# Performance work log

Hardware: AMD Instinct MI355X
Metric: run time of the kernel (lower is better)

The kernel has to match this reference:

```python
import jax, jax.numpy as jnp
import numpy as np

B, S, F_IN = 8, 4096, 256      # batch, frames, mel bins
C = 256                        # model_complexity (out_features of attention)
G = 8                          # n_heads (groups)
K = 31                         # w_size (local window, odd)
F_OUT = 88                     # output_features (piano keys)
PAD = (K - 1) // 2


def setup_inputs() -> dict:
    key = jax.random.key(0)
    ks = jax.random.split(key, 7)
    s = 0.05
    return {
        "spec": jax.random.normal(ks[0], (B, S, F_IN), jnp.float32),
        "W_q": jax.random.normal(ks[1], (F_IN, C), jnp.float32) * s,
        "W_k": jax.random.normal(ks[2], (F_IN, C), jnp.float32) * s,
        "W_v": jax.random.normal(ks[3], (F_IN, C), jnp.float32) * s,
        "rel": jax.random.normal(ks[4], (C, K), jnp.float32),
        "W_lin": jax.random.normal(ks[5], (C, F_OUT), jnp.float32) * s,
        "b_lin": jax.random.normal(ks[6], (F_OUT,), jnp.float32) * s,
    }


def reference(spec, W_q, W_k, W_v, rel, W_lin, b_lin):
    b, s, _ = spec.shape
    d = C // G  # per-head dim
    # QKV projections (no bias, as in the module)
    q = spec @ W_q                                             # [B,S,C]
    padded = jnp.pad(spec, ((0, 0), (PAD, PAD), (0, 0)))       # [B,S+2p,F]
    k = padded @ W_k                                           # [B,S+2p,C]
    v = padded @ W_v
    # unfold: window index [S,K]
    idx = jnp.arange(s)[:, None] + jnp.arange(K)[None, :]      # [S,K]
    kw = jnp.transpose(k[:, idx, :], (0, 1, 3, 2))             # [B,S,C,K]
    vw = jnp.transpose(v[:, idx, :], (0, 1, 3, 2))             # [B,S,C,K]
    kw = kw + rel                                              # positional bias [C,K]
    kw = kw.reshape(b, s, G, d, K)
    vw = vw.reshape(b, s, G, d, K)
    qh = q.reshape(b, s, G, d)
    energy = jnp.einsum('bsgd,bsgdk->bsgk', qh, kw)            # [B,S,G,K]
    attn = jax.nn.softmax(energy, axis=-1)                     # [B,S,G,K]
    out = jnp.einsum('bsgk,bsgdk->bsgd', attn, vw).reshape(b, s, C)
    frame_pred = jax.nn.sigmoid(out @ W_lin + b_lin)           # [B,S,F_OUT]
    return frame_pred, attn
```

## Files before the change

kernel.cpp:

```cpp
#include <hip/hip_runtime.h>
#include <hip/hip_bf16.h>
#include <math.h>

#define B_   8
#define S_   4096
#define FIN  256
#define C_   256
#define G_   8
#define D_   32
#define K_   31
#define PAD_ 15
#define FOUT 88

typedef __bf16 bf16;
typedef __attribute__((ext_vector_type(8))) __bf16 bf16x8;
typedef __attribute__((ext_vector_type(4))) __bf16 bf16x4;
typedef __attribute__((ext_vector_type(4))) float f32x4;

#define MFMA16(A, B, C) __builtin_amdgcn_mfma_f32_16x16x32_bf16(A, B, C, 0, 0, 0)

__global__ __launch_bounds__(256) void prep_all(
    const float* __restrict__ Wq, const float* __restrict__ Wk,
    const float* __restrict__ Wv, const float* __restrict__ Wl,
    const float* __restrict__ rel,
    bf16* __restrict__ bth, bf16* __restrict__ btl,
    bf16* __restrict__ wlh, bf16* __restrict__ wll,
    bf16* __restrict__ Vt,
    bf16* __restrict__ relH, bf16* __restrict__ relL)
{
    const int bid = blockIdx.x;
    const int t   = threadIdx.x;

    if (bid < 768) {
        const int w = bid >> 8;
        const int k = bid & 255;
        const float* W = (w == 0) ? Wq : (w == 1) ? Wk : Wv;
        const float x = W[(size_t)k * 256 + t];
        const bf16 h = (bf16)x;
        const size_t o = (size_t)w * 65536 + (size_t)t * 256 + k;
        bth[o] = h;
        btl[o] = (bf16)(x - (float)h);
    } else if (bid < 896) {
        const int k = (bid - 768) * 2 + (t >> 7);
        const int n = t & 127;
        const float x = (n < FOUT) ? Wl[(size_t)k * FOUT + n] : 0.f;
        const bf16 h = (bf16)x;
        wlh[(size_t)n * 256 + k] = h;
        wll[(size_t)n * 256 + k] = (bf16)(x - (float)h);
    } else if (bid < 1024) {
        const int idx = (bid - 896) * 256 + t;
        const int bd  = idx >> 4;
        const int pos = (idx & 15) * 4;
        const int off = (pos < 16) ? pos : 4096 + pos;
        bf16x4 z = {};
        *(bf16x4*)&Vt[(size_t)bd * 4160 + off] = z;
    } else {
        const int idx = (bid - 1024) * 256 + t;
        const int g = idx >> 10, k = (idx >> 5) & 31, d = idx & 31;
        const float v = (k < 31) ? rel[(size_t)(g * 32 + d) * 31 + k] : 0.f;
        const bf16 h = (bf16)v;
        relH[idx] = h;
        relL[idx] = (bf16)(v - (float)h);
    }
}

__device__ __forceinline__ void gload16(const bf16* g, bf16* l) {
    __builtin_amdgcn_global_load_lds(
        (const __attribute__((address_space(1))) void*)g,
        (__attribute__((address_space(3))) void*)l, 16, 0, 0);
}

__device__ __forceinline__ void stage_tile(const bf16* g, bf16* l, int t) {
    const int lg = ((t & 3) ^ ((t >> 3) & 3)) * 8;
    const int r0 = t >> 2;
    const int r1 = 64 + (t >> 2);
    const int u0 = (t & ~63) * 8;
    gload16(g + (size_t)r0 * 256 + lg, l + u0);
    gload16(g + (size_t)r1 * 256 + lg, l + u0 + 2048);
}

__device__ __forceinline__ bf16x8 frag_ld(const bf16* l, int r, int cl) {
    return *(const bf16x8*)&l[r * 32 + ((cl ^ ((r >> 1) & 3)) << 3)];
}

__global__ __launch_bounds__(256) void qkv_mfma(
    const float* __restrict__ spec,
    const bf16* __restrict__ bth, const bf16* __restrict__ btl,
    bf16* __restrict__ Qh, bf16* __restrict__ Ql,
    bf16* __restrict__ Kh, bf16* __restrict__ Kl,
    bf16* __restrict__ Vt)
{
    __shared__ bf16 lds[4 * 4096];

    const int t   = threadIdx.x;
    const int swz = ((blockIdx.x & 7) * 192) + (blockIdx.x >> 3);
    const int mt  = swz / 6, nt = swz % 6;
    const int wt  = nt >> 1;
    const int m0  = mt * 128, n0 = (nt & 1) * 128;
    const bool three = (wt < 2);

    const float* a_g = spec + (size_t)m0 * 256;
    const bf16* bh_g = bth + (size_t)wt * 65536 + (size_t)n0 * 256;
    const bf16* bl_g = btl + (size_t)wt * 65536 + (size_t)n0 * 256;

    const int ar  = t >> 1;
    const int ak  = (t & 1) * 16;
    const int as_ = (ar >> 1) & 3;
    const int cc0 = ak >> 3;
    bf16* AhW0 = lds +        ar * 32 + (( cc0      ^ as_) << 3);
    bf16* AhW1 = lds +        ar * 32 + (((cc0 + 1) ^ as_) << 3);
    bf16* AlW0 = lds + 4096 + ar * 32 + (( cc0      ^ as_) << 3);
    bf16* AlW1 = lds + 4096 + ar * 32 + (((cc0 + 1) ^ as_) << 3);
    const float* aRow = a_g + (size_t)ar * 256 + ak;

    const int lane = t & 63, wid = t >> 6;
    const int wr = (wid >> 1) * 64, wc = (wid & 1) * 64;
    const int fr = lane & 15, cl = lane >> 4;

    f32x4 acc[4][4];
#pragma unroll
    for (int m = 0; m < 4; ++m)
#pragma unroll
        for (int n = 0; n < 4; ++n)
            acc[m][n] = (f32x4){0.f, 0.f, 0.f, 0.f};

    for (int ks = 0; ks < 8; ++ks) {
        const int ko = ks * 32;

        const f32x4 a0 = *(const f32x4*)(aRow + ko);
        const f32x4 a1 = *(const f32x4*)(aRow + ko + 4);
        const f32x4 a2 = *(const f32x4*)(aRow + ko + 8);
        const f32x4 a3 = *(const f32x4*)(aRow + ko + 12);
        stage_tile(bh_g + ko, lds + 8192, t);
        stage_tile(bl_g + ko, lds + 12288, t);

        bf16x8 h0, h1, l0, l1;
#pragma unroll
        for (int j = 0; j < 4; ++j) {
            const bf16 x0 = (bf16)a0[j], x1 = (bf16)a1[j];
            const bf16 x2 = (bf16)a2[j], x3 = (bf16)a3[j];
            h0[j] = x0; h0[4 + j] = x1;
            h1[j] = x2; h1[4 + j] = x3;
            l0[j]     = (bf16)(a0[j] - (float)x0);
            l0[4 + j] = (bf16)(a1[j] - (float)x1);
            l1[j]     = (bf16)(a2[j] - (float)x2);
            l1[4 + j] = (bf16)(a3[j] - (float)x3);
        }
        *(bf16x8*)AhW0 = h0;
        *(bf16x8*)AhW1 = h1;
        if (three) {
            *(bf16x8*)AlW0 = l0;
            *(bf16x8*)AlW1 = l1;
        }
        __syncthreads();

        bf16x8 ah[4], bh8[4], bl8[4];
#pragma unroll
        for (int m = 0; m < 4; ++m) ah[m] = frag_ld(lds, wr + m * 16 + fr, cl);
#pragma unroll
        for (int n = 0; n < 4; ++n) {
            bh8[n] = frag_ld(lds + 8192,  wc + n * 16 + fr, cl);
            bl8[n] = frag_ld(lds + 12288, wc + n * 16 + fr, cl);
        }
#pragma unroll
        for (int m = 0; m < 4; ++m)
#pragma unroll
            for (int n = 0; n < 4; ++n) {
                acc[m][n] = MFMA16(ah[m], bh8[n], acc[m][n]);
                acc[m][n] = MFMA16(ah[m], bl8[n], acc[m][n]);
            }
        if (three) {
            bf16x8 al[4];
#pragma unroll
            for (int m = 0; m < 4; ++m) al[m] = frag_ld(lds + 4096, wr + m * 16 + fr, cl);
#pragma unroll
            for (int m = 0; m < 4; ++m)
#pragma unroll
                for (int n = 0; n < 4; ++n)
                    acc[m][n] = MFMA16(al[m], bh8[n], acc[m][n]);
        }
        __syncthreads();
    }

    if (wt < 2) {
        bf16* Oh = (wt == 0) ? Qh : Kh;
        bf16* Ol = (wt == 0) ? Ql : Kl;
#pragma unroll
        for (int m = 0; m < 4; ++m) {
            const int gr = m0 + wr + m * 16 + cl * 4;
#pragma unroll
            for (int n = 0; n < 4; ++n) {
                const int gc = n0 + wc + n * 16 + fr;
#pragma unroll
                for (int i = 0; i < 4; ++i) {
                    const float v = acc[m][n][i];
                    const bf16 hh = (bf16)v;
                    const size_t off = (size_t)(gr + i) * 256 + gc;
                    Oh[off] = hh;
                    Ol[off] = (bf16)(v - (float)hh);
                }
            }
        }
    } else {
#pragma unroll
        for (int m = 0; m < 4; ++m) {
            const int gr = m0 + wr + m * 16 + cl * 4;
            const int bb = gr >> 12, sr = gr & 4095;
#pragma unroll
            for (int n = 0; n < 4; ++n) {
                const int gc = n0 + wc + n * 16 + fr;
                bf16x4 pk;
#pragma unroll
                for (int i = 0; i < 4; ++i) pk[i] = (bf16)acc[m][n][i];
                *(bf16x4*)&Vt[(size_t)(bb * 256 + gc) * 4160 + 16 + sr] = pk;
            }
        }
    }
}

__global__ __launch_bounds__(256) void attn_mfma(
    const bf16* __restrict__ Qh, const bf16* __restrict__ Ql,
    const bf16* __restrict__ Kh, const bf16* __restrict__ Kl,
    const bf16* __restrict__ Vt,
    const bf16* __restrict__ relH, const bf16* __restrict__ relL,
    float* __restrict__ attn, bf16* __restrict__ Obf)
{
    __shared__ char ldsb[18432];

    const int t    = threadIdx.x;
    const int wid  = t >> 6;
    const int lane = t & 63;
    const int fr   = lane & 15;
    const int q    = lane >> 4;
    const int f7   = fr & 7;
    const int sl   = lane >> 2;
    const int jj   = lane & 3;

    const int bid2 = ((blockIdx.x & 7) << 8) | (blockIdx.x >> 3);
    const int sg0  = bid2 << 4;
    const int b    = sg0 >> 12;
    const int s0   = sg0 & 4095;

    float* Rbuf = (float*)(ldsb + wid * 4608);
    float* Pf32 = Rbuf;
    bf16*  Pbuf = (bf16*) (ldsb + wid * 4608 + 2304);

    {
        uint* p32 = (uint*)Pbuf;
#pragma unroll
        for (int j = 0; j < 9; ++j) p32[lane + 64 * j] = 0u;
    }

    const size_t rowQ = (size_t)(sg0 + fr) * 256;

#pragma unroll
    for (int h = 0; h < 2; ++h) {
        asm volatile("" ::: "memory");
        const int g   = wid * 2 + h;
        const int dof = g * 32 + q * 8;

        const bf16x8 qh8 = *(const bf16x8*)&Qh[rowQ + dof];
        const bf16x8 ql8 = *(const bf16x8*)&Ql[rowQ + dof];

        f32x4 e0, e1, e2;
#pragma unroll
        for (int tau = 0; tau < 3; ++tau) {
            const int trel = s0 - 16 + tau * 16 + fr;
            bf16x8 kh8 = {}, kl8 = {};
            if ((unsigned)trel < 4096u) {
                const size_t rk = ((size_t)(b << 12) + trel) * 256 + dof;
                kh8 = *(const bf16x8*)&Kh[rk];
                kl8 = *(const bf16x8*)&Kl[rk];
            }
            f32x4 a = (f32x4){0.f, 0.f, 0.f, 0.f};
            a = MFMA16(kh8, qh8, a);
            a = MFMA16(kh8, ql8, a);
            a = MFMA16(kl8, qh8, a);
            if (tau == 0) e0 = a; else if (tau == 1) e1 = a; else e2 = a;
        }

#pragma unroll
        for (int kap = 0; kap < 2; ++kap) {
            const size_t ro = (size_t)(g * 32 + kap * 16 + fr) * 32 + q * 8;
            const bf16x8 rh8 = *(const bf16x8*)&relH[ro];
            const bf16x8 rl8 = *(const bf16x8*)&relL[ro];
            f32x4 rc = (f32x4){0.f, 0.f, 0.f, 0.f};
            rc = MFMA16(rh8, qh8, rc);
            rc = MFMA16(rh8, ql8, rc);
            rc = MFMA16(rl8, qh8, rc);
#pragma unroll
            for (int r = 0; r < 4; ++r)
                Rbuf[(kap * 16 + q * 4 + r) * 18 + fr] = rc[r];
        }

        float ev[3][4];
        float mx = -3.0e38f;
#pragma unroll
        for (int tau = 0; tau < 3; ++tau) {
#pragma unroll
            for (int r = 0; r < 4; ++r) {
                const int rp = q * 4 + r;
                const int kk = tau * 16 + rp - fr - 1;
                const float eb = (tau == 0) ? e0[r] : (tau == 1) ? e1[r] : e2[r];
                float v = eb + Rbuf[(kk & 31) * 18 + fr];
                const bool valid = (tau == 1) || ((tau == 0) ? (rp > fr) : (rp < fr));
                v = valid ? v : -3.0e38f;
                ev[tau][r] = v;
                mx = fmaxf(mx, v);
            }
        }
        mx = fmaxf(mx, __shfl_xor(mx, 16));
        mx = fmaxf(mx, __shfl_xor(mx, 32));
        float sum = 0.f;
#pragma unroll
        for (int tau = 0; tau < 3; ++tau)
#pragma unroll
            for (int r = 0; r < 4; ++r) {
                const float p = __expf(ev[tau][r] - mx);
                ev[tau][r] = p;
                sum += p;
            }
        sum += __shfl_xor(sum, 16);
        sum += __shfl_xor(sum, 32);
        const float inv = 1.f / sum;

#pragma unroll
        for (int tau = 0; tau < 3; ++tau)
#pragma unroll
            for (int r = 0; r < 4; ++r) {
                const int rp = q * 4 + r;
                const int kk = tau * 16 + rp - fr - 1;
                const bool valid = (tau == 1) || ((tau == 0) ? (rp > fr) : (rp < fr));
                if (valid) {
                    const float p = ev[tau][r] * inv;
                    Pf32[fr * 36 + kk] = p;
                    const int tl = tau * 16 + rp;
                    Pbuf[fr * 72 + (((tl >> 3) ^ f7) << 3) + (tl & 7)] = (bf16)p;
                }
            }

        asm volatile("" ::: "memory");
        {
            float* arow = &attn[((size_t)(sg0 + sl) * 8 + g) * 31];
#pragma unroll
            for (int i = 0; i < 8; ++i) {
                const int k = jj + 4 * i;
                if (k < 31) arow[k] = Pf32[sl * 36 + k];
            }
        }

        asm volatile("" ::: "memory");
        const bf16x8 a0 = *(const bf16x8*)&Pbuf[fr * 72 + ((q ^ f7) << 3)];
        const bf16x8 a1 = *(const bf16x8*)&Pbuf[fr * 72 + (((4 + q) ^ f7) << 3)];
#pragma unroll
        for (int dl = 0; dl < 2; ++dl) {
            const size_t vrow = (size_t)(b * 256 + g * 32 + dl * 16 + fr) * 4160
                              + s0 + q * 8;
            const bf16x8 v0 = *(const bf16x8*)&Vt[vrow];
            const bf16x8 v1 = *(const bf16x8*)&Vt[vrow + 32];
            f32x4 o = (f32x4){0.f, 0.f, 0.f, 0.f};
            o = MFMA16(v0, a0, o);
            o = MFMA16(v1, a1, o);
            bf16x4 pk;
#pragma unroll
            for (int r = 0; r < 4; ++r) pk[r] = (bf16)o[r];
            *(bf16x4*)&Obf[(size_t)(sg0 + fr) * 256 + g * 32 + dl * 16 + (q << 2)] = pk;
        }
    }
}

__global__ __launch_bounds__(256) void frame_mfma(
    const bf16* __restrict__ O,
    const bf16* __restrict__ wlh, const bf16* __restrict__ wll,
    const float* __restrict__ bl, float* __restrict__ frame)
{
    __shared__ bf16 lds[3 * 4096];

    const int t  = threadIdx.x;
    const int m0 = blockIdx.x * 128;

    const bf16* a_g = O + (size_t)m0 * 256;

    const int lane = t & 63, wid = t >> 6;
    const int wr = (wid >> 1) * 64, wc = (wid & 1) * 64;
    const int fr = lane & 15, cl = lane >> 4;

    f32x4 acc[4][4];
#pragma unroll
    for (int m = 0; m < 4; ++m)
#pragma unroll
        for (int n = 0; n < 4; ++n)
            acc[m][n] = (f32x4){0.f, 0.f, 0.f, 0.f};

    for (int ks = 0; ks < 8; ++ks) {
        const int ko = ks * 32;
        stage_tile(a_g + ko, lds, t);
        stage_tile(wlh + ko, lds + 4096, t);
        stage_tile(wll + ko, lds + 8192, t);
        __syncthreads();

        bf16x8 ah[4], bh8[4], bl4[4];
#pragma unroll
        for (int m = 0; m < 4; ++m) ah[m] = frag_ld(lds, wr + m * 16 + fr, cl);
#pragma unroll
        for (int n = 0; n < 4; ++n) {
            bh8[n] = frag_ld(lds + 4096, wc + n * 16 + fr, cl);
            bl4[n] = frag_ld(lds + 8192, wc + n * 16 + fr, cl);
        }
#pragma unroll
        for (int m = 0; m < 4; ++m)
#pragma unroll
            for (int n = 0; n < 4; ++n) {
                acc[m][n] = MFMA16(ah[m], bh8[n], acc[m][n]);
                acc[m][n] = MFMA16(ah[m], bl4[n], acc[m][n]);
            }
        __syncthreads();
    }

#pragma unroll
    for (int m = 0; m < 4; ++m) {
        const int gr = m0 + wr + m * 16 + cl * 4;
#pragma unroll
        for (int n = 0; n < 4; ++n) {
            const int gc = wc + n * 16 + fr;
            if (gc < FOUT) {
                const float bb = bl[gc];
#pragma unroll
                for (int i = 0; i < 4; ++i) {
                    const float x = acc[m][n][i] + bb;
                    frame[(size_t)(gr + i) * FOUT + gc] = 1.f / (1.f + __expf(-x));
                }
            }
        }
    }
}

extern "C" void kernel_launch(void* const* d_in, const int* in_sizes, int n_in,
                              void* d_out, int out_size, void* d_ws, size_t ws_size,
                              hipStream_t stream) {
    (void)in_sizes; (void)n_in; (void)out_size; (void)ws_size;
    const float* spec = (const float*)d_in[0];
    const float* Wq   = (const float*)d_in[1];
    const float* Wk   = (const float*)d_in[2];
    const float* Wv   = (const float*)d_in[3];
    const float* rel  = (const float*)d_in[4];
    const float* Wl   = (const float*)d_in[5];
    const float* bl   = (const float*)d_in[6];

    float* frame = (float*)d_out;
    float* attn  = frame + (size_t)B_ * S_ * FOUT;

    bf16* bth  = (bf16*)((char*)d_out + 33554432);
    bf16* btl  = bth + 3 * 65536;
    bf16* relH = (bf16*)d_out;
    bf16* relL = relH + 8192;

    bf16* Qh  = (bf16*)d_ws;
    bf16* Ql  = Qh + (size_t)8388608;
    bf16* Kh  = Ql + (size_t)8388608;
    bf16* Kl  = Kh + (size_t)8388608;
    bf16* Vt  = Kl + (size_t)8388608;
    bf16* wlh = Vt + (size_t)8 * 256 * 4160;
    bf16* wll = wlh + 128 * 256;

    prep_all  <<<dim3(1056), 256, 0, stream>>>(Wq, Wk, Wv, Wl, rel,
                                               bth, btl, wlh, wll, Vt, relH, relL);
    qkv_mfma  <<<dim3(1536), 256, 0, stream>>>(spec, bth, btl, Qh, Ql, Kh, Kl, Vt);
    attn_mfma <<<dim3(2048), 256, 0, stream>>>(Qh, Ql, Kh, Kl, Vt, relH, relL, attn, Qh);
    frame_mfma<<<dim3(256),  256, 0, stream>>>(Qh, wlh, wll, bl, frame);
}
```

Before: 111.9 us.

## Fuse frame projection into attention kernel and double-buffer QKV GEMM staging

```diff
diff --git a/kernel.cpp b/kernel.cpp
--- a/kernel.cpp
+++ b/kernel.cpp
@@ -90,7 +90,7 @@
     bf16* __restrict__ Kh, bf16* __restrict__ Kl,
     bf16* __restrict__ Vt)
 {
-    __shared__ bf16 lds[4 * 4096];
+    __shared__ bf16 lds[6 * 4096];
 
     const int t   = threadIdx.x;
     const int swz = ((blockIdx.x & 7) * 192) + (blockIdx.x >> 3);
@@ -124,15 +124,28 @@
         for (int n = 0; n < 4; ++n)
             acc[m][n] = (f32x4){0.f, 0.f, 0.f, 0.f};
 
+    stage_tile(bh_g, lds + 8192, t);
+    stage_tile(bl_g, lds + 12288, t);
+    f32x4 a0 = *(const f32x4*)(aRow);
+    f32x4 a1 = *(const f32x4*)(aRow + 4);
+    f32x4 a2 = *(const f32x4*)(aRow + 8);
+    f32x4 a3 = *(const f32x4*)(aRow + 12);
+
     for (int ks = 0; ks < 8; ++ks) {
-        const int ko = ks * 32;
-
-        const f32x4 a0 = *(const f32x4*)(aRow + ko);
-        const f32x4 a1 = *(const f32x4*)(aRow + ko + 4);
-        const f32x4 a2 = *(const f32x4*)(aRow + ko + 8);
-        const f32x4 a3 = *(const f32x4*)(aRow + ko + 12);
-        stage_tile(bh_g + ko, lds + 8192, t);
-        stage_tile(bl_g + ko, lds + 12288, t);
+        const int cur = ks & 1;
+        bf16* Bcur = lds + 8192 + cur * 8192;
+
+        f32x4 n0_, n1_, n2_, n3_;
+        if (ks < 7) {
+            bf16* Bnxt = lds + 8192 + (cur ^ 1) * 8192;
+            const int ko2 = (ks + 1) * 32;
+            stage_tile(bh_g + ko2, Bnxt, t);
+            stage_tile(bl_g + ko2, Bnxt + 4096, t);
+            n0_ = *(const f32x4*)(aRow + ko2);
+            n1_ = *(const f32x4*)(aRow + ko2 + 4);
+            n2_ = *(const f32x4*)(aRow + ko2 + 8);
+            n3_ = *(const f32x4*)(aRow + ko2 + 12);
+        }
 
         bf16x8 h0, h1, l0, l1;
 #pragma unroll
@@ -152,15 +165,17 @@
             *(bf16x8*)AlW0 = l0;
             *(bf16x8*)AlW1 = l1;
         }
-        __syncthreads();
+
+        asm volatile("s_waitcnt vmcnt(8) lgkmcnt(0)" ::: "memory");
+        __builtin_amdgcn_s_barrier();
 
         bf16x8 ah[4], bh8[4], bl8[4];
 #pragma unroll
         for (int m = 0; m < 4; ++m) ah[m] = frag_ld(lds, wr + m * 16 + fr, cl);
 #pragma unroll
         for (int n = 0; n < 4; ++n) {
-            bh8[n] = frag_ld(lds + 8192,  wc + n * 16 + fr, cl);
-            bl8[n] = frag_ld(lds + 12288, wc + n * 16 + fr, cl);
+            bh8[n] = frag_ld(Bcur,        wc + n * 16 + fr, cl);
+            bl8[n] = frag_ld(Bcur + 4096, wc + n * 16 + fr, cl);
         }
 #pragma unroll
         for (int m = 0; m < 4; ++m)
@@ -179,7 +194,11 @@
                 for (int n = 0; n < 4; ++n)
                     acc[m][n] = MFMA16(al[m], bh8[n], acc[m][n]);
         }
-        __syncthreads();
+
+        if (ks < 7) {
+            __builtin_amdgcn_s_barrier();
+            a0 = n0_; a1 = n1_; a2 = n2_; a3 = n3_;
+        }
     }
 
     if (wt < 2) {
@@ -223,9 +242,12 @@
     const bf16* __restrict__ Kh, const bf16* __restrict__ Kl,
     const bf16* __restrict__ Vt,
     const bf16* __restrict__ relH, const bf16* __restrict__ relL,
-    float* __restrict__ attn, bf16* __restrict__ Obf)
+    const bf16* __restrict__ wlh, const bf16* __restrict__ wll,
+    const float* __restrict__ blin,
+    float* __restrict__ attn, float* __restrict__ frame)
 {
     __shared__ char ldsb[18432];
+    __shared__ bf16 ldsO[16 * 264];
 
     const int t    = threadIdx.x;
     const int wid  = t >> 6;
@@ -350,8 +372,8 @@
         }
 
         asm volatile("" ::: "memory");
-        const bf16x8 a0 = *(const bf16x8*)&Pbuf[fr * 72 + ((q ^ f7) << 3)];
-        const bf16x8 a1 = *(const bf16x8*)&Pbuf[fr * 72 + (((4 + q) ^ f7) << 3)];
+        const bf16x8 pa0 = *(const bf16x8*)&Pbuf[fr * 72 + ((q ^ f7) << 3)];
+        const bf16x8 pa1 = *(const bf16x8*)&Pbuf[fr * 72 + (((4 + q) ^ f7) << 3)];
 #pragma unroll
         for (int dl = 0; dl < 2; ++dl) {
             const size_t vrow = (size_t)(b * 256 + g * 32 + dl * 16 + fr) * 4160
@@ -359,76 +381,42 @@
             const bf16x8 v0 = *(const bf16x8*)&Vt[vrow];
             const bf16x8 v1 = *(const bf16x8*)&Vt[vrow + 32];
             f32x4 o = (f32x4){0.f, 0.f, 0.f, 0.f};
-            o = MFMA16(v0, a0, o);
-            o = MFMA16(v1, a1, o);
+            o = MFMA16(v0, pa0, o);
+            o = MFMA16(v1, pa1, o);
             bf16x4 pk;
 #pragma unroll
             for (int r = 0; r < 4; ++r) pk[r] = (bf16)o[r];
-            *(bf16x4*)&Obf[(size_t)(sg0 + fr) * 256 + g * 32 + dl * 16 + (q << 2)] = pk;
-        }
-    }
-}
-
-__global__ __launch_bounds__(256) void frame_mfma(
-    const bf16* __restrict__ O,
-    const bf16* __restrict__ wlh, const bf16* __restrict__ wll,
-    const float* __restrict__ bl, float* __restrict__ frame)
-{
-    __shared__ bf16 lds[3 * 4096];
-
-    const int t  = threadIdx.x;
-    const int m0 = blockIdx.x * 128;
-
-    const bf16* a_g = O + (size_t)m0 * 256;
-
-    const int lane = t & 63, wid = t >> 6;
-    const int wr = (wid >> 1) * 64, wc = (wid & 1) * 64;
-    const int fr = lane & 15, cl = lane >> 4;
-
-    f32x4 acc[4][4];
-#pragma unroll
-    for (int m = 0; m < 4; ++m)
-#pragma unroll
-        for (int n = 0; n < 4; ++n)
-            acc[m][n] = (f32x4){0.f, 0.f, 0.f, 0.f};
-
-    for (int ks = 0; ks < 8; ++ks) {
-        const int ko = ks * 32;
-        stage_tile(a_g + ko, lds, t);
-        stage_tile(wlh + ko, lds + 4096, t);
-        stage_tile(wll + ko, lds + 8192, t);
-        __syncthreads();
-
-        bf16x8 ah[4], bh8[4], bl4[4];
-#pragma unroll
-        for (int m = 0; m < 4; ++m) ah[m] = frag_ld(lds, wr + m * 16 + fr, cl);
-#pragma unroll
-        for (int n = 0; n < 4; ++n) {
-            bh8[n] = frag_ld(lds + 4096, wc + n * 16 + fr, cl);
-            bl4[n] = frag_ld(lds + 8192, wc + n * 16 + fr, cl);
-        }
-#pragma unroll
-        for (int m = 0; m < 4; ++m)
-#pragma unroll
-            for (int n = 0; n < 4; ++n) {
-                acc[m][n] = MFMA16(ah[m], bh8[n], acc[m][n]);
-                acc[m][n] = MFMA16(ah[m], bl4[n], acc[m][n]);
-            }
-        __syncthreads();
-    }
-
-#pragma unroll
-    for (int m = 0; m < 4; ++m) {
-        const int gr = m0 + wr + m * 16 + cl * 4;
-#pragma unroll
-        for (int n = 0; n < 4; ++n) {
-            const int gc = wc + n * 16 + fr;
+            *(bf16x4*)&ldsO[fr * 264 + g * 32 + dl * 16 + q * 4] = pk;
+        }
+    }
+
+    __syncthreads();
+
+    if (wid < 3) {
+        f32x4 fac[2];
+        fac[0] = (f32x4){0.f, 0.f, 0.f, 0.f};
+        fac[1] = (f32x4){0.f, 0.f, 0.f, 0.f};
+#pragma unroll
+        for (int ks = 0; ks < 8; ++ks) {
+            const bf16x8 ao = *(const bf16x8*)&ldsO[fr * 264 + ks * 32 + q * 8];
+#pragma unroll
+            for (int n = 0; n < 2; ++n) {
+                const int nc = wid * 32 + n * 16 + fr;
+                const bf16x8 bh8 = *(const bf16x8*)&wlh[(size_t)nc * 256 + ks * 32 + q * 8];
+                const bf16x8 bl8 = *(const bf16x8*)&wll[(size_t)nc * 256 + ks * 32 + q * 8];
+                fac[n] = MFMA16(ao, bh8, fac[n]);
+                fac[n] = MFMA16(ao, bl8, fac[n]);
+            }
+        }
+#pragma unroll
+        for (int n = 0; n < 2; ++n) {
+            const int gc = wid * 32 + n * 16 + fr;
             if (gc < FOUT) {
-                const float bb = bl[gc];
+                const float bb = blin[gc];
 #pragma unroll
                 for (int i = 0; i < 4; ++i) {
-                    const float x = acc[m][n][i] + bb;
-                    frame[(size_t)(gr + i) * FOUT + gc] = 1.f / (1.f + __expf(-x));
+                    const float x = fac[n][i] + bb;
+                    frame[(size_t)(sg0 + q * 4 + i) * FOUT + gc] = 1.f / (1.f + __expf(-x));
                 }
             }
         }
@@ -452,20 +440,20 @@
 
     bf16* bth  = (bf16*)((char*)d_out + 33554432);
     bf16* btl  = bth + 3 * 65536;
-    bf16* relH = (bf16*)d_out;
+
+    bf16* Qh   = (bf16*)d_ws;
+    bf16* Ql   = Qh + (size_t)8388608;
+    bf16* Kh   = Ql + (size_t)8388608;
+    bf16* Kl   = Kh + (size_t)8388608;
+    bf16* Vt   = Kl + (size_t)8388608;
+    bf16* wlh  = Vt + (size_t)8 * 256 * 4160;
+    bf16* wll  = wlh + 128 * 256;
+    bf16* relH = wll + 128 * 256;
     bf16* relL = relH + 8192;
 
-    bf16* Qh  = (bf16*)d_ws;
-    bf16* Ql  = Qh + (size_t)8388608;
-    bf16* Kh  = Ql + (size_t)8388608;
-    bf16* Kl  = Kh + (size_t)8388608;
-    bf16* Vt  = Kl + (size_t)8388608;
-    bf16* wlh = Vt + (size_t)8 * 256 * 4160;
-    bf16* wll = wlh + 128 * 256;
-
-    prep_all  <<<dim3(1056), 256, 0, stream>>>(Wq, Wk, Wv, Wl, rel,
-                                               bth, btl, wlh, wll, Vt, relH, relL);
-    qkv_mfma  <<<dim3(1536), 256, 0, stream>>>(spec, bth, btl, Qh, Ql, Kh, Kl, Vt);
-    attn_mfma <<<dim3(2048), 256, 0, stream>>>(Qh, Ql, Kh, Kl, Vt, relH, relL, attn, Qh);
-    frame_mfma<<<dim3(256),  256, 0, stream>>>(Qh, wlh, wll, bl, frame);
-}
+    prep_all <<<dim3(1056), 256, 0, stream>>>(Wq, Wk, Wv, Wl, rel,
+                                              bth, btl, wlh, wll, Vt, relH, relL);
+    qkv_mfma <<<dim3(1536), 256, 0, stream>>>(spec, bth, btl, Qh, Ql, Kh, Kl, Vt);
+    attn_mfma<<<dim3(2048), 256, 0, stream>>>(Qh, Ql, Kh, Kl, Vt, relH, relL,
+                                              wlh, wll, bl, attn, frame);
+}
```

Result: no change. 111.6 us (-0.3%).
